# Kernel tuning notes

Measured on AMD Instinct MI355X. Metric: run time of the kernel, lower is better.

## Reference

```python
import jax, jax.numpy as jnp
import numpy as np

N = 100000
E = 1600000
H = 128       # hidden_channels
HEADS = 8
HD = H // HEADS  # head_dim = 16


def setup_inputs() -> dict:
    key = jax.random.key(0)
    ks = jax.random.split(key, 10)
    x = jax.random.normal(ks[0], (N, H), dtype=jnp.float32)
    gap_edge_index = jax.random.randint(ks[1], (2, E), 0, N, dtype=jnp.int64)
    s = 1.0 / np.sqrt(H)
    Wq = jax.random.normal(ks[2], (H, H), dtype=jnp.float32) * s
    bq = jnp.zeros((H,), dtype=jnp.float32)
    Wk = jax.random.normal(ks[3], (H, H), dtype=jnp.float32) * s
    bk = jnp.zeros((H,), dtype=jnp.float32)
    Wv = jax.random.normal(ks[4], (H, H), dtype=jnp.float32) * s
    bv = jnp.zeros((H,), dtype=jnp.float32)
    Wo = jax.random.normal(ks[5], (H, H), dtype=jnp.float32) * s
    bo = jnp.zeros((H,), dtype=jnp.float32)
    return {"x": x, "gap_edge_index": gap_edge_index,
            "Wq": Wq, "bq": bq, "Wk": Wk, "bk": bk,
            "Wv": Wv, "bv": bv, "Wo": Wo, "bo": bo}


def reference(x, gap_edge_index, Wq, bq, Wk, bk, Wv, bv, Wo, bo):
    n = x.shape[0]
    q = (x @ Wq + bq).reshape(n, HEADS, HD)
    k = (x @ Wk + bk).reshape(n, HEADS, HD)
    v = (x @ Wv + bv).reshape(n, HEADS, HD)
    src, dst = gap_edge_index[0], gap_edge_index[1]
    # per-edge, per-head scores: [E, heads]
    scores = jnp.einsum('ehd,ehd->eh', q[dst], k[src]) / jnp.sqrt(jnp.float32(HD))
    # NOTE: original softmaxes over ALL edges (dim=0), not per-dst segment
    w = jax.nn.softmax(scores, axis=0)
    # scatter-add weighted v[src] into dst: [N, heads, head_dim]
    attended = jax.ops.segment_sum(w[:, :, None] * v[src], dst, num_segments=n)
    attended = attended.reshape(n, HEADS * HD)
    return x + attended @ Wo + bo
```

## Files before the change

kernel.cpp:

```cpp
#include <hip/hip_runtime.h>
#include <cstdint>
#include <cstddef>

#define N_NODES 100000
#define E_EDGES 1600000
#define HCH 128
#define NHEADS 8
#define HDIM 16

typedef unsigned int uint;
typedef unsigned short ushort;
typedef unsigned char uchar;
typedef __attribute__((ext_vector_type(8))) short short8;
typedef __attribute__((ext_vector_type(4))) float floatx4;
typedef __attribute__((ext_vector_type(2))) float floatx2;

constexpr int GTILES = (N_NODES + 63) / 64;

__device__ __forceinline__ ushort f2bf(float f) {
    uint u = __float_as_uint(f);
    u = (u + 0x7fff + ((u >> 16) & 1)) >> 16;
    return (ushort)u;
}
__device__ __forceinline__ float bflo(uint p) { return __uint_as_float(p << 16); }
__device__ __forceinline__ float bfhi(uint p) { return __uint_as_float(p & 0xffff0000u); }

constexpr int BSHIFT = 8;
constexpr int NBUCK  = ((N_NODES - 1) >> BSHIFT) + 1;
constexpr int S1_GRID = 256;
constexpr int S1_CH   = (E_EDGES + S1_GRID - 1) / S1_GRID;
constexpr int S2_CAP  = 6144;
constexpr int FU_BLOCKS = 2048;
constexpr int FU_GROUPS = FU_BLOCKS * 16;

__global__ __launch_bounds__(256) void prep_w(
    const float* __restrict__ Wq, const float* __restrict__ Wk,
    const float* __restrict__ Wv, const float* __restrict__ Wo,
    ushort* __restrict__ wall, int* __restrict__ bucket_total)
{
    const int t = threadIdx.x;
    if (blockIdx.x == 0) {
        for (int b = t; b < NBUCK + 1; b += 256) bucket_total[b] = 0;
    }
    int r = blockIdx.x * 16 + (t >> 4);
    int k0 = (t & 15) * 8;
    const float* W;
    if (r < 128)      W = Wq;
    else if (r < 256) W = Wk;
    else if (r < 384) W = Wv;
    else              W = Wo;
    int n = r & 127;
    uint4 u;
    u.x = (uint)f2bf(W[(size_t)(k0 + 0) * HCH + n]) | ((uint)f2bf(W[(size_t)(k0 + 1) * HCH + n]) << 16);
    u.y = (uint)f2bf(W[(size_t)(k0 + 2) * HCH + n]) | ((uint)f2bf(W[(size_t)(k0 + 3) * HCH + n]) << 16);
    u.z = (uint)f2bf(W[(size_t)(k0 + 4) * HCH + n]) | ((uint)f2bf(W[(size_t)(k0 + 5) * HCH + n]) << 16);
    u.w = (uint)f2bf(W[(size_t)(k0 + 6) * HCH + n]) | ((uint)f2bf(W[(size_t)(k0 + 7) * HCH + n]) << 16);
    *(uint4*)(wall + (size_t)r * HCH + k0) = u;
}

__global__ __launch_bounds__(256) void bucket_hist(
    const int* __restrict__ dst, int* __restrict__ bucket_total)
{
    __shared__ int cnt[NBUCK];
    const int t = threadIdx.x;
    for (int b = t; b < NBUCK; b += 256) cnt[b] = 0;
    __syncthreads();
    const int e0 = blockIdx.x * S1_CH;
    const int n = min(S1_CH, E_EDGES - e0);
    for (int i = t; i < n; i += 256)
        atomicAdd(&cnt[dst[e0 + i] >> BSHIFT], 1);
    __syncthreads();
    for (int b = t; b < NBUCK; b += 256)
        if (cnt[b]) atomicAdd(&bucket_total[b], cnt[b]);
}

__global__ __launch_bounds__(512) void bucket_scan(
    const int* __restrict__ bucket_total, int* __restrict__ bucket_start,
    int* __restrict__ bucket_cursor, int* __restrict__ offsets)
{
    __shared__ int s[512];
    const int t = threadIdx.x;
    int v = (t < NBUCK) ? bucket_total[t] : 0;
    s[t] = v;
    __syncthreads();
    for (int off = 1; off < 512; off <<= 1) {
        int a = (t >= off) ? s[t - off] : 0;
        __syncthreads();
        s[t] += a;
        __syncthreads();
    }
    int excl = s[t] - v;
    if (t < NBUCK) { bucket_start[t] = excl; bucket_cursor[t] = excl; }
    if (t == 0) { bucket_start[NBUCK] = E_EDGES; offsets[N_NODES] = E_EDGES; }
}

__global__ __launch_bounds__(256) void mega_qkv_scatter(
    const float* __restrict__ A, const ushort* __restrict__ wall,
    const float* __restrict__ bq, const float* __restrict__ bk, const float* __restrict__ bv,
    uchar* __restrict__ qe, uchar* __restrict__ kb, uchar* __restrict__ vb,
    const int* __restrict__ src, const int* __restrict__ dst,
    int* __restrict__ bucket_cursor, uint* __restrict__ tmp,
    int M)
{
    __shared__ __align__(16) char sm[34816 + 17408];
    const int t = threadIdx.x;
    const int bid = blockIdx.x;

    if (bid < S1_GRID) {
        int* cnt = (int*)sm;
        for (int b = t; b < NBUCK; b += 256) cnt[b] = 0;
        __syncthreads();
        const int e0 = bid * S1_CH;
        const int n = min(S1_CH, E_EDGES - e0);
        for (int i = t; i < n; i += 256)
            atomicAdd(&cnt[dst[e0 + i] >> BSHIFT], 1);
        __syncthreads();
        for (int b = t; b < NBUCK; b += 256) {
            int c = cnt[b];
            cnt[b] = c ? atomicAdd(&bucket_cursor[b], c) : 0;
        }
        __syncthreads();
        for (int i = t; i < n; i += 256) {
            int d = dst[e0 + i];
            int s = src[e0 + i];
            int pos = atomicAdd(&cnt[d >> BSHIFT], 1);
            tmp[pos] = (uint)s | ((uint)(d & 255) << 24);
        }
        return;
    }

    ushort (*Wt)[136] = (ushort(*)[136])sm;
    ushort (*As)[136] = (ushort(*)[136])(sm + 34816);
    ushort (*Cs)[136] = (ushort(*)[136])(sm + 34816);

    const int b = bid - S1_GRID;
    const int mode = b % 3;
    const int tile0 = b / 3;
    const float* bias;
    uchar* outp;
    if (mode == 0)      { bias = bq; outp = qe; }
    else if (mode == 1) { bias = bk; outp = kb; }
    else                { bias = bv; outp = vb; }

#pragma unroll
    for (int i = 0; i < 8; i++) {
        int p = t + i * 256;
        int row = p >> 4, k0 = (p & 15) * 8;
        *(uint4*)(&Wt[row][k0]) =
            *(const uint4*)(wall + ((size_t)(mode * 128 + row)) * HCH + k0);
    }

    const int lane = t & 63;
    const int w = t >> 6;
    const int m_l = lane & 15;
    const int q_l = lane >> 4;

    const int eu = t & 15;
    const float4 eb0 = *(const float4*)(bias + eu * 8);
    const float4 eb1 = *(const float4*)(bias + eu * 8 + 4);
    const int arow = t >> 5, ac4 = t & 31;

    float4 a4[8];
    {
        const int mb = tile0 * 64;
#pragma unroll
        for (int i = 0; i < 8; i++) {
            int row = arow + i * 8;
            int g = mb + row;
            a4[i] = make_float4(0.f, 0.f, 0.f, 0.f);
            if (g < M) a4[i] = *(const float4*)(A + (size_t)g * HCH + ac4 * 4);
        }
    }

    for (int tile = tile0; tile < GTILES; tile += 256) {
        const int mb = tile * 64;
#pragma unroll
        for (int i = 0; i < 8; i++) {
            uint lo = (uint)f2bf(a4[i].x) | ((uint)f2bf(a4[i].y) << 16);
            uint hi = (uint)f2bf(a4[i].z) | ((uint)f2bf(a4[i].w) << 16);
            *(uint2*)(&As[arow + i * 8][ac4 * 4]) = make_uint2(lo, hi);
        }
        const int ntile = tile + 256;
        if (ntile < GTILES) {
            const int nmb = ntile * 64;
#pragma unroll
            for (int i = 0; i < 8; i++) {
                int g = nmb + arow + i * 8;
                float4 v = make_float4(0.f, 0.f, 0.f, 0.f);
                if (g < M) v = *(const float4*)(A + (size_t)g * HCH + ac4 * 4);
                a4[i] = v;
            }
        }
        __syncthreads();

        floatx4 acc[8];
#pragma unroll
        for (int tl = 0; tl < 8; tl++) acc[tl] = (floatx4){0.f, 0.f, 0.f, 0.f};
#pragma unroll
        for (int ks = 0; ks < 4; ks++) {
            short8 af = *(const short8*)(&As[w * 16 + m_l][ks * 32 + q_l * 8]);
#pragma unroll
            for (int tl = 0; tl < 8; tl++) {
                short8 bf = *(const short8*)(&Wt[tl * 16 + m_l][ks * 32 + q_l * 8]);
                acc[tl] = __builtin_amdgcn_mfma_f32_16x16x32_bf16(af, bf, acc[tl], 0, 0, 0);
            }
        }
        __syncthreads();

#pragma unroll
        for (int tl = 0; tl < 8; tl++)
#pragma unroll
            for (int r = 0; r < 4; r++)
                Cs[w * 16 + q_l * 4 + r][tl * 16 + m_l] = f2bf(acc[tl][r]);
        __syncthreads();

#pragma unroll
        for (int i = 0; i < 4; i++) {
            int row = (t >> 4) + i * 16;
            int g = mb + row;
            if (g < M) {
                uint4 c = *(const uint4*)(&Cs[row][eu * 8]);
                int r0 = __builtin_amdgcn_cvt_pk_fp8_f32(bflo(c.x) + eb0.x, bfhi(c.x) + eb0.y, 0, false);
                r0 = __builtin_amdgcn_cvt_pk_fp8_f32(bflo(c.y) + eb0.z, bfhi(c.y) + eb0.w, r0, true);
                int r1 = __builtin_amdgcn_cvt_pk_fp8_f32(bflo(c.z) + eb1.x, bfhi(c.z) + eb1.y, 0, false);
                r1 = __builtin_amdgcn_cvt_pk_fp8_f32(bflo(c.w) + eb1.z, bfhi(c.w) + eb1.w, r1, true);
                *(uint2*)(outp + (size_t)g * 128 + eu * 8) = make_uint2((uint)r0, (uint)r1);
            }
        }
        __syncthreads();
    }
}

__global__ __launch_bounds__(256) void sort_scatter2(
    const uint* __restrict__ tmp, const int* __restrict__ bucket_start,
    int* __restrict__ psrc, int* __restrict__ offsets)
{
    __shared__ uint le[S2_CAP];
    __shared__ int cnt[256];
    __shared__ int s[256];
    __shared__ int cur[256];
    const int t = threadIdx.x;
    const int b = blockIdx.x;
    const int bstart = bucket_start[b];
    const int n = bucket_start[b + 1] - bstart;
    cnt[t] = 0;
    __syncthreads();
    for (int i = t; i < n; i += 256) {
        uint e = tmp[bstart + i];
        if (i < S2_CAP) le[i] = e;
        atomicAdd(&cnt[e >> 24], 1);
    }
    __syncthreads();
    int v = cnt[t];
    s[t] = v;
    __syncthreads();
    for (int off = 1; off < 256; off <<= 1) {
        int a = (t >= off) ? s[t - off] : 0;
        __syncthreads();
        s[t] += a;
        __syncthreads();
    }
    int excl = s[t] - v;
    int node = (b << BSHIFT) + t;
    if (node < N_NODES) offsets[node] = bstart + excl;
    cur[t] = excl;
    __syncthreads();
    for (int i = t; i < n; i += 256) {
        uint e = (i < S2_CAP) ? le[i] : tmp[bstart + i];
        int pos = bstart + atomicAdd(&cur[e >> 24], 1);
        psrc[pos] = (int)(e & 0x1FFFFu);
    }
}

__device__ __forceinline__ float edge_w(
    uint2 e, floatx2 q0, floatx2 q1, floatx2 q2, floatx2 q3)
{
    floatx2 dp = q0 * __builtin_amdgcn_cvt_pk_f32_fp8((int)e.x, false);
    dp += q1 * __builtin_amdgcn_cvt_pk_f32_fp8((int)e.x, true);
    dp += q2 * __builtin_amdgcn_cvt_pk_f32_fp8((int)e.y, false);
    dp += q3 * __builtin_amdgcn_cvt_pk_f32_fp8((int)e.y, true);
    float p = dp.x + dp.y;
    p += __shfl_xor(p, 1);
    return __expf(p * 0.25f);
}
__device__ __forceinline__ void edge_acc(
    uint2 e, float wgt, floatx2& a01, floatx2& a23, floatx2& a45, floatx2& a67)
{
    floatx2 wv = {wgt, wgt};
    a01 += wv * __builtin_amdgcn_cvt_pk_f32_fp8((int)e.x, false);
    a23 += wv * __builtin_amdgcn_cvt_pk_f32_fp8((int)e.x, true);
    a45 += wv * __builtin_amdgcn_cvt_pk_f32_fp8((int)e.y, false);
    a67 += wv * __builtin_amdgcn_cvt_pk_f32_fp8((int)e.y, true);
}

#define LOADQ(S, base) do { \
    int jj1 = min((base) + 1, end - 1); \
    int jj2 = min((base) + 2, end - 1); \
    int jj3 = min((base) + 3, end - 1); \
    int u0 = psrc[(base)], u1 = psrc[jj1], u2 = psrc[jj2], u3 = psrc[jj3]; \
    k##S##0 = *(const uint2*)(kb + (size_t)u0 * 128 + sub * 8); \
    k##S##1 = *(const uint2*)(kb + (size_t)u1 * 128 + sub * 8); \
    k##S##2 = *(const uint2*)(kb + (size_t)u2 * 128 + sub * 8); \
    k##S##3 = *(const uint2*)(kb + (size_t)u3 * 128 + sub * 8); \
    v##S##0 = *(const uint2*)(vb + (size_t)u0 * 128 + sub * 8); \
    v##S##1 = *(const uint2*)(vb + (size_t)u1 * 128 + sub * 8); \
    v##S##2 = *(const uint2*)(vb + (size_t)u2 * 128 + sub * 8); \
    v##S##3 = *(const uint2*)(vb + (size_t)u3 * 128 + sub * 8); \
} while (0)

#define COMPQ(S, base) do { \
    float w0 = edge_w(k##S##0, q0, q1, q2, q3); \
    float w1 = edge_w(k##S##1, q0, q1, q2, q3); \
    float w2 = edge_w(k##S##2, q0, q1, q2, q3); \
    float w3 = edge_w(k##S##3, q0, q1, q2, q3); \
    if ((base) + 1 >= end) w1 = 0.f; \
    if ((base) + 2 >= end) w2 = 0.f; \
    if ((base) + 3 >= end) w3 = 0.f; \
    lsum += w0 + w1 + w2 + w3; \
    edge_acc(v##S##0, w0, a01, a23, a45, a67); \
    edge_acc(v##S##1, w1, a01, a23, a45, a67); \
    edge_acc(v##S##2, w2, a01, a23, a45, a67); \
    edge_acc(v##S##3, w3, a01, a23, a45, a67); \
} while (0)

__global__ __launch_bounds__(256) void edge_fused(
    const uchar* __restrict__ qe, const uchar* __restrict__ kb, const uchar* __restrict__ vb,
    const int* __restrict__ psrc, const int* __restrict__ offsets,
    ushort* __restrict__ attended, float* __restrict__ block_l)
{
    const int t = threadIdx.x;
    const int sub = t & 15;
    const int gg0 = blockIdx.x * 16 + (t >> 4);

    float lsum = 0.f;

    for (int d = gg0; d < N_NODES; d += FU_GROUPS) {
        const int start = offsets[d];
        const int end   = offsets[d + 1];

        uint2 qw = *(const uint2*)(qe + (size_t)d * 128 + sub * 8);
        floatx2 q0 = __builtin_amdgcn_cvt_pk_f32_fp8((int)qw.x, false);
        floatx2 q1 = __builtin_amdgcn_cvt_pk_f32_fp8((int)qw.x, true);
        floatx2 q2 = __builtin_amdgcn_cvt_pk_f32_fp8((int)qw.y, false);
        floatx2 q3 = __builtin_amdgcn_cvt_pk_f32_fp8((int)qw.y, true);

        floatx2 a01 = {0.f, 0.f}, a23 = {0.f, 0.f}, a45 = {0.f, 0.f}, a67 = {0.f, 0.f};

        uint2 kA0, kA1, kA2, kA3, vA0, vA1, vA2, vA3;
        uint2 kB0, kB1, kB2, kB3, vB0, vB1, vB2, vB3;

        int i = start;
        if (i < end) {
            LOADQ(A, i);
            while (true) {
                if (i + 4 < end) LOADQ(B, i + 4);
                COMPQ(A, i);
                i += 4;
                if (i >= end) break;
                if (i + 4 < end) LOADQ(A, i + 4);
                COMPQ(B, i);
                i += 4;
                if (i >= end) break;
            }
        }

        uint4 o;
        o.x = (uint)f2bf(a01.x) | ((uint)f2bf(a01.y) << 16);
        o.y = (uint)f2bf(a23.x) | ((uint)f2bf(a23.y) << 16);
        o.z = (uint)f2bf(a45.x) | ((uint)f2bf(a45.y) << 16);
        o.w = (uint)f2bf(a67.x) | ((uint)f2bf(a67.y) << 16);
        *(uint4*)(attended + (size_t)d * HCH + sub * 8) = o;
    }

    __shared__ float sl[256];
    sl[t] = lsum;
    __syncthreads();
    if (t < 8) {
        float L = 0.f;
        for (int base = 0; base < 256; base += 16)
            L += sl[base + 2 * t] + sl[base + 2 * t + 1];
        block_l[blockIdx.x * 8 + t] = 0.5f * L;
    }
}

__global__ __launch_bounds__(256) void gemm_out(
    const ushort* __restrict__ A, const ushort* __restrict__ wall,
    const float* __restrict__ bias, const float* __restrict__ res,
    const float* __restrict__ block_l,
    float* __restrict__ C, int M)
{
    __shared__ __align__(16) char sm[34816 + 17408];
    ushort (*Wt)[136] = (ushort(*)[136])sm;
    ushort (*As)[136] = (ushort(*)[136])(sm + 34816);
    ushort (*Cs)[136] = (ushort(*)[136])(sm + 34816);
    __shared__ float invl_s[8];
    __shared__ float sl[256];

    const int t = threadIdx.x;

    {
        float l = 0.f;
        for (int i = t; i < FU_BLOCKS * 8; i += 256) l += block_l[i];
        sl[t] = l;
        __syncthreads();
        if (t < 8) {
            float L = 0.f;
            for (int j = t; j < 256; j += 8) L += sl[j];
            invl_s[t] = 1.0f / L;
        }
    }

#pragma unroll
    for (int i = 0; i < 8; i++) {
        int p = t + i * 256;
        int row = p >> 4, k0 = (p & 15) * 8;
        *(uint4*)(&Wt[row][k0]) =
            *(const uint4*)(wall + ((size_t)(384 + row)) * HCH + k0);
    }
    __syncthreads();

    const int lane = t & 63;
    const int w = t >> 6;
    const int m_l = lane & 15;
    const int q_l = lane >> 4;

    const int arow = t >> 5, acu2 = t & 31;
    const float invl_a = invl_s[acu2 >> 2];
    const int eu = t & 31;
    const float4 eb = *(const float4*)(bias + eu * 4);

    uint2 a2[8];
    {
        const int mb = blockIdx.x * 64;
#pragma unroll
        for (int i = 0; i < 8; i++) {
            int g = mb + arow + i * 8;
            a2[i] = make_uint2(0, 0);
            if (g < M) a2[i] = *(const uint2*)(A + (size_t)g * HCH + acu2 * 4);
        }
    }

    for (int tile = blockIdx.x; tile < GTILES; tile += 768) {
        const int mb = tile * 64;
#pragma unroll
        for (int i = 0; i < 8; i++) {
            float f0 = bflo(a2[i].x) * invl_a, f1 = bfhi(a2[i].x) * invl_a;
            float f2 = bflo(a2[i].y) * invl_a, f3 = bfhi(a2[i].y) * invl_a;
            uint lo = (uint)f2bf(f0) | ((uint)f2bf(f1) << 16);
            uint hi = (uint)f2bf(f2) | ((uint)f2bf(f3) << 16);
            *(uint2*)(&As[arow + i * 8][acu2 * 4]) = make_uint2(lo, hi);
        }
        const int ntile = tile + 768;
        if (ntile < GTILES) {
            const int nmb = ntile * 64;
#pragma unroll
            for (int i = 0; i < 8; i++) {
                int g = nmb + arow + i * 8;
                uint2 v = make_uint2(0, 0);
                if (g < M) v = *(const uint2*)(A + (size_t)g * HCH + acu2 * 4);
                a2[i] = v;
            }
        }
        __syncthreads();

        floatx4 acc[8];
#pragma unroll
        for (int tl = 0; tl < 8; tl++) acc[tl] = (floatx4){0.f, 0.f, 0.f, 0.f};
#pragma unroll
        for (int ks = 0; ks < 4; ks++) {
            short8 af = *(const short8*)(&As[w * 16 + m_l][ks * 32 + q_l * 8]);
#pragma unroll
            for (int tl = 0; tl < 8; tl++) {
                short8 bf = *(const short8*)(&Wt[tl * 16 + m_l][ks * 32 + q_l * 8]);
                acc[tl] = __builtin_amdgcn_mfma_f32_16x16x32_bf16(af, bf, acc[tl], 0, 0, 0);
            }
        }
        __syncthreads();

#pragma unroll
        for (int tl = 0; tl < 8; tl++)
#pragma unroll
            for (int r = 0; r < 4; r++)
                Cs[w * 16 + q_l * 4 + r][tl * 16 + m_l] = f2bf(acc[tl][r]);
        __syncthreads();

#pragma unroll
        for (int i = 0; i < 8; i++) {
            int row = (t >> 5) + i * 8;
            int g = mb + row;
            if (g < M) {
                uint2 c = *(const uint2*)(&Cs[row][eu * 4]);
                float4 r4 = *(const float4*)(res + (size_t)g * HCH + eu * 4);
                float4 o;
                o.x = bflo(c.x) + eb.x + r4.x;
                o.y = bfhi(c.x) + eb.y + r4.y;
                o.z = bflo(c.y) + eb.z + r4.z;
                o.w = bfhi(c.y) + eb.w + r4.w;
                *(float4*)(C + (size_t)g * HCH + eu * 4) = o;
            }
        }
        __syncthreads();
    }
}

extern "C" void kernel_launch(void* const* d_in, const int* in_sizes, int n_in,
                              void* d_out, int out_size, void* d_ws, size_t ws_size,
                              hipStream_t stream)
{
    const float* x  = (const float*)d_in[0];
    const int* eidx = (const int*)d_in[1];
    const float* Wq = (const float*)d_in[2];
    const float* bq = (const float*)d_in[3];
    const float* Wk = (const float*)d_in[4];
    const float* bk = (const float*)d_in[5];
    const float* Wv = (const float*)d_in[6];
    const float* bv = (const float*)d_in[7];
    const float* Wo = (const float*)d_in[8];
    const float* bo = (const float*)d_in[9];
    float* out = (float*)d_out;

    char* ws = (char*)d_ws;
    constexpr size_t SZ_F8  = (size_t)N_NODES * HCH;
    constexpr size_t SZ_ATT = (size_t)N_NODES * HCH * 2;
    constexpr size_t SZ_PS  = (size_t)E_EDGES * sizeof(int);
    constexpr size_t SZ_TMP = (size_t)E_EDGES * sizeof(uint);
    size_t off = 0;
    uchar* qe = (uchar*)(ws + off); off += SZ_F8;
    uchar* kb = (uchar*)(ws + off); off += SZ_F8;
    uchar* vb = (uchar*)(ws + off); off += SZ_F8;
    ushort* attended = (ushort*)(ws + off); off += SZ_ATT;
    int*    psrc     = (int*)(ws + off);    off += SZ_PS;
    uint*   tmp      = (uint*)(ws + off);   off += SZ_TMP;
    int*    offsets  = (int*)(ws + off);    off += ((size_t)N_NODES + 1) * 4 + 8;
    int*    bucket_total  = (int*)(ws + off); off += (NBUCK + 1) * 4;
    int*    bucket_start  = (int*)(ws + off); off += (NBUCK + 1) * 4;
    int*    bucket_cursor = (int*)(ws + off); off += (NBUCK + 1) * 4;
    float*  block_l   = (float*)(ws + off); off += (size_t)FU_BLOCKS * 8 * sizeof(float);
    ushort* wall = (ushort*)(ws + off); off += (size_t)512 * HCH * 2;
    const int* src = eidx;
    const int* dst = eidx + E_EDGES;

    dim3 blk(256);

    prep_w<<<32, blk, 0, stream>>>(Wq, Wk, Wv, Wo, wall, bucket_total);
    bucket_hist<<<S1_GRID, blk, 0, stream>>>(dst, bucket_total);
    bucket_scan<<<1, 512, 0, stream>>>(bucket_total, bucket_start, bucket_cursor, offsets);

    mega_qkv_scatter<<<S1_GRID + 768, blk, 0, stream>>>(
        x, wall, bq, bk, bv, qe, kb, vb, src, dst, bucket_cursor, tmp, N_NODES);

    sort_scatter2<<<NBUCK, blk, 0, stream>>>(tmp, bucket_start, psrc, offsets);

    edge_fused<<<FU_BLOCKS, blk, 0, stream>>>(qe, kb, vb, psrc, offsets, attended, block_l);

    gemm_out<<<768, blk, 0, stream>>>(attended, wall, bo, x, block_l, out, N_NODES);
}
```

Before: 295.9 us.

## Hold weight fragments in registers, store attended as fp8, merge prep kernels

The two GEMM kernels now keep each wave's weight column fragments in registers instead of staging the full weight matrix in LDS. This halves shared memory per block, so more blocks can be resident, and it removes one barrier per tile. Grid sizes are raised to match. The attended intermediate is written as fp8 instead of bf16, which halves its write and read traffic. The exp gets a constant shift to keep fp8 values in range. The weight-prep and histogram kernels are merged into one launch with a memset. All of this risks precision loss from fp8 rounding of the attention output.

```diff
diff --git a/kernel.cpp b/kernel.cpp
--- a/kernel.cpp
+++ b/kernel.cpp
@@ -32,17 +32,32 @@
 constexpr int S2_CAP  = 6144;
 constexpr int FU_BLOCKS = 2048;
 constexpr int FU_GROUPS = FU_BLOCKS * 16;
-
-__global__ __launch_bounds__(256) void prep_w(
+constexpr int GQ_BLOCKS = 1278;
+constexpr int GQ_STRIDE = 426;
+constexpr int GO_BLOCKS = 1024;
+
+__global__ __launch_bounds__(256) void prep_hist(
     const float* __restrict__ Wq, const float* __restrict__ Wk,
     const float* __restrict__ Wv, const float* __restrict__ Wo,
-    ushort* __restrict__ wall, int* __restrict__ bucket_total)
+    ushort* __restrict__ wall,
+    const int* __restrict__ dst, int* __restrict__ bucket_total)
 {
     const int t = threadIdx.x;
-    if (blockIdx.x == 0) {
-        for (int b = t; b < NBUCK + 1; b += 256) bucket_total[b] = 0;
-    }
-    int r = blockIdx.x * 16 + (t >> 4);
+    const int bid = blockIdx.x;
+    if (bid < S1_GRID) {
+        __shared__ int cnt[NBUCK];
+        for (int b = t; b < NBUCK; b += 256) cnt[b] = 0;
+        __syncthreads();
+        const int e0 = bid * S1_CH;
+        const int n = min(S1_CH, E_EDGES - e0);
+        for (int i = t; i < n; i += 256)
+            atomicAdd(&cnt[dst[e0 + i] >> BSHIFT], 1);
+        __syncthreads();
+        for (int b = t; b < NBUCK; b += 256)
+            if (cnt[b]) atomicAdd(&bucket_total[b], cnt[b]);
+        return;
+    }
+    int r = (bid - S1_GRID) * 16 + (t >> 4);
     int k0 = (t & 15) * 8;
     const float* W;
     if (r < 128)      W = Wq;
@@ -58,22 +73,6 @@
     *(uint4*)(wall + (size_t)r * HCH + k0) = u;
 }
 
-__global__ __launch_bounds__(256) void bucket_hist(
-    const int* __restrict__ dst, int* __restrict__ bucket_total)
-{
-    __shared__ int cnt[NBUCK];
-    const int t = threadIdx.x;
-    for (int b = t; b < NBUCK; b += 256) cnt[b] = 0;
-    __syncthreads();
-    const int e0 = blockIdx.x * S1_CH;
-    const int n = min(S1_CH, E_EDGES - e0);
-    for (int i = t; i < n; i += 256)
-        atomicAdd(&cnt[dst[e0 + i] >> BSHIFT], 1);
-    __syncthreads();
-    for (int b = t; b < NBUCK; b += 256)
-        if (cnt[b]) atomicAdd(&bucket_total[b], cnt[b]);
-}
-
 __global__ __launch_bounds__(512) void bucket_scan(
     const int* __restrict__ bucket_total, int* __restrict__ bucket_start,
     int* __restrict__ bucket_cursor, int* __restrict__ offsets)
@@ -102,7 +101,7 @@
     int* __restrict__ bucket_cursor, uint* __restrict__ tmp,
     int M)
 {
-    __shared__ __align__(16) char sm[34816 + 17408];
+    __shared__ __align__(16) char sm[34816];
     const int t = threadIdx.x;
     const int bid = blockIdx.x;
 
@@ -129,9 +128,8 @@
         return;
     }
 
-    ushort (*Wt)[136] = (ushort(*)[136])sm;
-    ushort (*As)[136] = (ushort(*)[136])(sm + 34816);
-    ushort (*Cs)[136] = (ushort(*)[136])(sm + 34816);
+    ushort (*As)[136] = (ushort(*)[136])sm;
+    ushort (*Cs)[136] = (ushort(*)[136])(sm + 17408);
 
     const int b = bid - S1_GRID;
     const int mode = b % 3;
@@ -142,19 +140,21 @@
     else if (mode == 1) { bias = bk; outp = kb; }
     else                { bias = bv; outp = vb; }
 
-#pragma unroll
-    for (int i = 0; i < 8; i++) {
-        int p = t + i * 256;
-        int row = p >> 4, k0 = (p & 15) * 8;
-        *(uint4*)(&Wt[row][k0]) =
-            *(const uint4*)(wall + ((size_t)(mode * 128 + row)) * HCH + k0);
-    }
-
     const int lane = t & 63;
     const int w = t >> 6;
     const int m_l = lane & 15;
     const int q_l = lane >> 4;
 
+    short8 wfr[2][4];
+    {
+        const ushort* wb = wall + (size_t)(mode * 128 + 2 * w * 16 + m_l) * HCH + q_l * 8;
+#pragma unroll
+        for (int tlj = 0; tlj < 2; tlj++)
+#pragma unroll
+            for (int ks = 0; ks < 4; ks++)
+                wfr[tlj][ks] = *(const short8*)(wb + (size_t)tlj * 16 * HCH + ks * 32);
+    }
+
     const int eu = t & 15;
     const float4 eb0 = *(const float4*)(bias + eu * 8);
     const float4 eb1 = *(const float4*)(bias + eu * 8 + 4);
@@ -165,14 +165,13 @@
         const int mb = tile0 * 64;
 #pragma unroll
         for (int i = 0; i < 8; i++) {
-            int row = arow + i * 8;
-            int g = mb + row;
+            int g = mb + arow + i * 8;
             a4[i] = make_float4(0.f, 0.f, 0.f, 0.f);
             if (g < M) a4[i] = *(const float4*)(A + (size_t)g * HCH + ac4 * 4);
         }
     }
 
-    for (int tile = tile0; tile < GTILES; tile += 256) {
+    for (int tile = tile0; tile < GTILES; tile += GQ_STRIDE) {
         const int mb = tile * 64;
 #pragma unroll
         for (int i = 0; i < 8; i++) {
@@ -180,7 +179,7 @@
             uint hi = (uint)f2bf(a4[i].z) | ((uint)f2bf(a4[i].w) << 16);
             *(uint2*)(&As[arow + i * 8][ac4 * 4]) = make_uint2(lo, hi);
         }
-        const int ntile = tile + 256;
+        const int ntile = tile + GQ_STRIDE;
         if (ntile < GTILES) {
             const int nmb = ntile * 64;
 #pragma unroll
@@ -193,25 +192,28 @@
         }
         __syncthreads();
 
-        floatx4 acc[8];
-#pragma unroll
-        for (int tl = 0; tl < 8; tl++) acc[tl] = (floatx4){0.f, 0.f, 0.f, 0.f};
+        floatx4 acc[4][2];
+#pragma unroll
+        for (int ms = 0; ms < 4; ms++) {
+            acc[ms][0] = (floatx4){0.f, 0.f, 0.f, 0.f};
+            acc[ms][1] = (floatx4){0.f, 0.f, 0.f, 0.f};
+        }
 #pragma unroll
         for (int ks = 0; ks < 4; ks++) {
-            short8 af = *(const short8*)(&As[w * 16 + m_l][ks * 32 + q_l * 8]);
-#pragma unroll
-            for (int tl = 0; tl < 8; tl++) {
-                short8 bf = *(const short8*)(&Wt[tl * 16 + m_l][ks * 32 + q_l * 8]);
-                acc[tl] = __builtin_amdgcn_mfma_f32_16x16x32_bf16(af, bf, acc[tl], 0, 0, 0);
-            }
-        }
-        __syncthreads();
-
-#pragma unroll
-        for (int tl = 0; tl < 8; tl++)
-#pragma unroll
-            for (int r = 0; r < 4; r++)
-                Cs[w * 16 + q_l * 4 + r][tl * 16 + m_l] = f2bf(acc[tl][r]);
+#pragma unroll
+            for (int ms = 0; ms < 4; ms++) {
+                short8 af = *(const short8*)(&As[ms * 16 + m_l][ks * 32 + q_l * 8]);
+                acc[ms][0] = __builtin_amdgcn_mfma_f32_16x16x32_bf16(af, wfr[0][ks], acc[ms][0], 0, 0, 0);
+                acc[ms][1] = __builtin_amdgcn_mfma_f32_16x16x32_bf16(af, wfr[1][ks], acc[ms][1], 0, 0, 0);
+            }
+        }
+#pragma unroll
+        for (int ms = 0; ms < 4; ms++)
+#pragma unroll
+            for (int tlj = 0; tlj < 2; tlj++)
+#pragma unroll
+                for (int r = 0; r < 4; r++)
+                    Cs[ms * 16 + q_l * 4 + r][(2 * w + tlj) * 16 + m_l] = f2bf(acc[ms][tlj][r]);
         __syncthreads();
 
 #pragma unroll
@@ -281,7 +283,7 @@
     dp += q3 * __builtin_amdgcn_cvt_pk_f32_fp8((int)e.y, true);
     float p = dp.x + dp.y;
     p += __shfl_xor(p, 1);
-    return __expf(p * 0.25f);
+    return __expf(p * 0.25f - 2.772588722f);
 }
 __device__ __forceinline__ void edge_acc(
     uint2 e, float wgt, floatx2& a01, floatx2& a23, floatx2& a45, floatx2& a67)
@@ -326,7 +328,7 @@
 __global__ __launch_bounds__(256) void edge_fused(
     const uchar* __restrict__ qe, const uchar* __restrict__ kb, const uchar* __restrict__ vb,
     const int* __restrict__ psrc, const int* __restrict__ offsets,
-    ushort* __restrict__ attended, float* __restrict__ block_l)
+    uchar* __restrict__ attended, float* __restrict__ block_l)
 {
     const int t = threadIdx.x;
     const int sub = t & 15;
@@ -364,12 +366,11 @@
             }
         }
 
-        uint4 o;
-        o.x = (uint)f2bf(a01.x) | ((uint)f2bf(a01.y) << 16);
-        o.y = (uint)f2bf(a23.x) | ((uint)f2bf(a23.y) << 16);
-        o.z = (uint)f2bf(a45.x) | ((uint)f2bf(a45.y) << 16);
-        o.w = (uint)f2bf(a67.x) | ((uint)f2bf(a67.y) << 16);
-        *(uint4*)(attended + (size_t)d * HCH + sub * 8) = o;
+        int r0 = __builtin_amdgcn_cvt_pk_fp8_f32(a01.x, a01.y, 0, false);
+        r0 = __builtin_amdgcn_cvt_pk_fp8_f32(a23.x, a23.y, r0, true);
+        int r1 = __builtin_amdgcn_cvt_pk_fp8_f32(a45.x, a45.y, 0, false);
+        r1 = __builtin_amdgcn_cvt_pk_fp8_f32(a67.x, a67.y, r1, true);
+        *(uint2*)(attended + (size_t)d * 128 + sub * 8) = make_uint2((uint)r0, (uint)r1);
     }
 
     __shared__ float sl[256];
@@ -384,15 +385,14 @@
 }
 
 __global__ __launch_bounds__(256) void gemm_out(
-    const ushort* __restrict__ A, const ushort* __restrict__ wall,
+    const uchar* __restrict__ A, const ushort* __restrict__ wall,
     const float* __restrict__ bias, const float* __restrict__ res,
     const float* __restrict__ block_l,
     float* __restrict__ C, int M)
 {
-    __shared__ __align__(16) char sm[34816 + 17408];
-    ushort (*Wt)[136] = (ushort(*)[136])sm;
-    ushort (*As)[136] = (ushort(*)[136])(sm + 34816);
-    ushort (*Cs)[136] = (ushort(*)[136])(sm + 34816);
+    __shared__ __align__(16) char sm[34816];
+    ushort (*As)[136] = (ushort(*)[136])sm;
+    ushort (*Cs)[136] = (ushort(*)[136])(sm + 17408);
     __shared__ float invl_s[8];
     __shared__ float sl[256];
 
@@ -408,80 +408,90 @@
             for (int j = t; j < 256; j += 8) L += sl[j];
             invl_s[t] = 1.0f / L;
         }
-    }
-
-#pragma unroll
-    for (int i = 0; i < 8; i++) {
-        int p = t + i * 256;
-        int row = p >> 4, k0 = (p & 15) * 8;
-        *(uint4*)(&Wt[row][k0]) =
-            *(const uint4*)(wall + ((size_t)(384 + row)) * HCH + k0);
-    }
-    __syncthreads();
+        __syncthreads();
+    }
 
     const int lane = t & 63;
     const int w = t >> 6;
     const int m_l = lane & 15;
     const int q_l = lane >> 4;
 
-    const int arow = t >> 5, acu2 = t & 31;
-    const float invl_a = invl_s[acu2 >> 2];
+    short8 wfr[2][4];
+    {
+        const ushort* wb = wall + (size_t)(384 + 2 * w * 16 + m_l) * HCH + q_l * 8;
+#pragma unroll
+        for (int tlj = 0; tlj < 2; tlj++)
+#pragma unroll
+            for (int ks = 0; ks < 4; ks++)
+                wfr[tlj][ks] = *(const short8*)(wb + (size_t)tlj * 16 * HCH + ks * 32);
+    }
+
+    const int arow = t >> 4, au = t & 15;
+    const float invl_a = invl_s[au >> 1];
     const int eu = t & 31;
     const float4 eb = *(const float4*)(bias + eu * 4);
 
-    uint2 a2[8];
+    uint2 a2[4];
     {
         const int mb = blockIdx.x * 64;
 #pragma unroll
-        for (int i = 0; i < 8; i++) {
-            int g = mb + arow + i * 8;
+        for (int i = 0; i < 4; i++) {
+            int g = mb + arow + i * 16;
             a2[i] = make_uint2(0, 0);
-            if (g < M) a2[i] = *(const uint2*)(A + (size_t)g * HCH + acu2 * 4);
-        }
-    }
-
-    for (int tile = blockIdx.x; tile < GTILES; tile += 768) {
+            if (g < M) a2[i] = *(const uint2*)(A + (size_t)g * 128 + au * 8);
+        }
+    }
+
+    for (int tile = blockIdx.x; tile < GTILES; tile += GO_BLOCKS) {
         const int mb = tile * 64;
 #pragma unroll
-        for (int i = 0; i < 8; i++) {
-            float f0 = bflo(a2[i].x) * invl_a, f1 = bfhi(a2[i].x) * invl_a;
-            float f2 = bflo(a2[i].y) * invl_a, f3 = bfhi(a2[i].y) * invl_a;
-            uint lo = (uint)f2bf(f0) | ((uint)f2bf(f1) << 16);
-            uint hi = (uint)f2bf(f2) | ((uint)f2bf(f3) << 16);
-            *(uint2*)(&As[arow + i * 8][acu2 * 4]) = make_uint2(lo, hi);
-        }
-        const int ntile = tile + 768;
+        for (int i = 0; i < 4; i++) {
+            floatx2 f01 = __builtin_amdgcn_cvt_pk_f32_fp8((int)a2[i].x, false);
+            floatx2 f23 = __builtin_amdgcn_cvt_pk_f32_fp8((int)a2[i].x, true);
+            floatx2 f45 = __builtin_amdgcn_cvt_pk_f32_fp8((int)a2[i].y, false);
+            floatx2 f67 = __builtin_amdgcn_cvt_pk_f32_fp8((int)a2[i].y, true);
+            uint4 o;
+            o.x = (uint)f2bf(f01.x * invl_a) | ((uint)f2bf(f01.y * invl_a) << 16);
+            o.y = (uint)f2bf(f23.x * invl_a) | ((uint)f2bf(f23.y * invl_a) << 16);
+            o.z = (uint)f2bf(f45.x * invl_a) | ((uint)f2bf(f45.y * invl_a) << 16);
+            o.w = (uint)f2bf(f67.x * invl_a) | ((uint)f2bf(f67.y * invl_a) << 16);
+            *(uint4*)(&As[arow + i * 16][au * 8]) = o;
+        }
+        const int ntile = tile + GO_BLOCKS;
         if (ntile < GTILES) {
             const int nmb = ntile * 64;
 #pragma unroll
-            for (int i = 0; i < 8; i++) {
-                int g = nmb + arow + i * 8;
+            for (int i = 0; i < 4; i++) {
+                int g = nmb + arow + i * 16;
                 uint2 v = make_uint2(0, 0);
-                if (g < M) v = *(const uint2*)(A + (size_t)g * HCH + acu2 * 4);
+                if (g < M) v = *(const uint2*)(A + (size_t)g * 128 + au * 8);
                 a2[i] = v;
             }
         }
         __syncthreads();
 
-        floatx4 acc[8];
-#pragma unroll
-        for (int tl = 0; tl < 8; tl++) acc[tl] = (floatx4){0.f, 0.f, 0.f, 0.f};
+        floatx4 acc[4][2];
+#pragma unroll
+        for (int ms = 0; ms < 4; ms++) {
+            acc[ms][0] = (floatx4){0.f, 0.f, 0.f, 0.f};
+            acc[ms][1] = (floatx4){0.f, 0.f, 0.f, 0.f};
+        }
 #pragma unroll
         for (int ks = 0; ks < 4; ks++) {
-            short8 af = *(const short8*)(&As[w * 16 + m_l][ks * 32 + q_l * 8]);
-#pragma unroll
-            for (int tl = 0; tl < 8; tl++) {
-                short8 bf = *(const short8*)(&Wt[tl * 16 + m_l][ks * 32 + q_l * 8]);
-                acc[tl] = __builtin_amdgcn_mfma_f32_16x16x32_bf16(af, bf, acc[tl], 0, 0, 0);
-            }
-        }
-        __syncthreads();
-
-#pragma unroll
-        for (int tl = 0; tl < 8; tl++)
-#pragma unroll
-            for (int r = 0; r < 4; r++)
-                Cs[w * 16 + q_l * 4 + r][tl * 16 + m_l] = f2bf(acc[tl][r]);
+#pragma unroll
+            for (int ms = 0; ms < 4; ms++) {
+                short8 af = *(const short8*)(&As[ms * 16 + m_l][ks * 32 + q_l * 8]);
+                acc[ms][0] = __builtin_amdgcn_mfma_f32_16x16x32_bf16(af, wfr[0][ks], acc[ms][0], 0, 0, 0);
+                acc[ms][1] = __builtin_amdgcn_mfma_f32_16x16x32_bf16(af, wfr[1][ks], acc[ms][1], 0, 0, 0);
+            }
+        }
+#pragma unroll
+        for (int ms = 0; ms < 4; ms++)
+#pragma unroll
+            for (int tlj = 0; tlj < 2; tlj++)
+#pragma unroll
+                for (int r = 0; r < 4; r++)
+                    Cs[ms * 16 + q_l * 4 + r][(2 * w + tlj) * 16 + m_l] = f2bf(acc[ms][tlj][r]);
         __syncthreads();
 
 #pragma unroll
@@ -521,14 +531,13 @@
 
     char* ws = (char*)d_ws;
     constexpr size_t SZ_F8  = (size_t)N_NODES * HCH;
-    constexpr size_t SZ_ATT = (size_t)N_NODES * HCH * 2;
     constexpr size_t SZ_PS  = (size_t)E_EDGES * sizeof(int);
     constexpr size_t SZ_TMP = (size_t)E_EDGES * sizeof(uint);
     size_t off = 0;
     uchar* qe = (uchar*)(ws + off); off += SZ_F8;
     uchar* kb = (uchar*)(ws + off); off += SZ_F8;
     uchar* vb = (uchar*)(ws + off); off += SZ_F8;
-    ushort* attended = (ushort*)(ws + off); off += SZ_ATT;
+    uchar* attended = (uchar*)(ws + off); off += SZ_F8;
     int*    psrc     = (int*)(ws + off);    off += SZ_PS;
     uint*   tmp      = (uint*)(ws + off);   off += SZ_TMP;
     int*    offsets  = (int*)(ws + off);    off += ((size_t)N_NODES + 1) * 4 + 8;
@@ -542,16 +551,16 @@
 
     dim3 blk(256);
 
-    prep_w<<<32, blk, 0, stream>>>(Wq, Wk, Wv, Wo, wall, bucket_total);
-    bucket_hist<<<S1_GRID, blk, 0, stream>>>(dst, bucket_total);
+    hipMemsetAsync(bucket_total, 0, (NBUCK + 1) * 4, stream);
+    prep_hist<<<S1_GRID + 32, blk, 0, stream>>>(Wq, Wk, Wv, Wo, wall, dst, bucket_total);
     bucket_scan<<<1, 512, 0, stream>>>(bucket_total, bucket_start, bucket_cursor, offsets);
 
-    mega_qkv_scatter<<<S1_GRID + 768, blk, 0, stream>>>(
+    mega_qkv_scatter<<<S1_GRID + GQ_BLOCKS, blk, 0, stream>>>(
         x, wall, bq, bk, bv, qe, kb, vb, src, dst, bucket_cursor, tmp, N_NODES);
 
     sort_scatter2<<<NBUCK, blk, 0, stream>>>(tmp, bucket_start, psrc, offsets);
 
     edge_fused<<<FU_BLOCKS, blk, 0, stream>>>(qe, kb, vb, psrc, offsets, attended, block_l);
 
-    gemm_out<<<768, blk, 0, stream>>>(attended, wall, bo, x, block_l, out, N_NODES);
-}
+    gemm_out<<<GO_BLOCKS, blk, 0, stream>>>(attended, wall, bo, x, block_l, out, N_NODES);
+}
```

New measurement: 292.7 us. About the same (-1.1%).
